# Kernel tuning notes

Measured on AMD Instinct MI355X. Metric: run time of the kernel, lower is better.

The kernel has to match this reference:

```python
import jax, jax.numpy as jnp
import numpy as np

B, N, H, W = 64, 21, 128, 128
MSE_WEIGHT = 1.0
SOFT_PCK_WEIGHT = 1.0


def setup_inputs() -> dict:
    key = jax.random.key(0)
    k1, k2, k3 = jax.random.split(key, 3)
    pred_heatmaps = jax.random.uniform(k1, (B, N, H, W), dtype=jnp.float32)
    gt_heatmaps = jax.random.uniform(k2, (B, N, H, W), dtype=jnp.float32)
    # pixel coordinates (x, y) in [0, W) x [0, H)
    gt_keypoints_2D = jax.random.uniform(k3, (B, N, 2), dtype=jnp.float32) * jnp.array([W, H], dtype=jnp.float32)
    return {"pred_heatmaps": pred_heatmaps, "gt_heatmaps": gt_heatmaps, "gt_keypoints_2D": gt_keypoints_2D}


def reference(pred_heatmaps, gt_heatmaps, gt_keypoints_2D):
    b, n, h, w = pred_heatmaps.shape
    # MSE over all elements
    mse_loss = jnp.mean((pred_heatmaps - gt_heatmaps) ** 2)
    # Vectorized keypoint gather: clamp coords, truncate-cast (matches torch .long())
    x = jnp.clip(gt_keypoints_2D[..., 0], 0, w - 1).astype(jnp.int32)  # (B, N)
    y = jnp.clip(gt_keypoints_2D[..., 1], 0, h - 1).astype(jnp.int32)  # (B, N)
    bi = jnp.arange(b)[:, None]
    ni = jnp.arange(n)[None, :]
    pred_vals = pred_heatmaps[bi, ni, y, x]  # (B, N)
    soft_pck_loss = jnp.sum((1.0 - pred_vals) ** 2) / (b * n)
    total_loss = MSE_WEIGHT * mse_loss + SOFT_PCK_WEIGHT * soft_pck_loss
    return (total_loss, mse_loss, soft_pck_loss)
```

## Files before the change

### kernel.cpp

```cpp
#include <hip/hip_runtime.h>

#define BB 64
#define NN 21
#define HH 128
#define WW 128
static constexpr long long TOT_ELEMS = (long long)BB * NN * HH * WW;
static constexpr int NV4 = (int)(TOT_ELEMS / 4);
static constexpr int NKP = BB * NN;

__global__ __launch_bounds__(256) void combined_loss_kernel(
    const float4* __restrict__ pred4,
    const float4* __restrict__ gt4,
    const float*  __restrict__ pred,
    const float*  __restrict__ kp,
    float* __restrict__ acc)
{
    const int tid    = blockIdx.x * blockDim.x + threadIdx.x;
    const int stride = gridDim.x * blockDim.x;

    float s = 0.0f;
    for (int i = tid; i < NV4; i += stride) {
        float4 p = pred4[i];
        float4 g = gt4[i];
        float d0 = p.x - g.x;
        float d1 = p.y - g.y;
        float d2 = p.z - g.z;
        float d3 = p.w - g.w;
        s += d0 * d0 + d1 * d1 + d2 * d2 + d3 * d3;
    }

    float s2 = 0.0f;
    if (tid < NKP) {
        float px = kp[2 * tid + 0];
        float py = kp[2 * tid + 1];
        int xi = (int)fminf(fmaxf(px, 0.0f), (float)(WW - 1));
        int yi = (int)fminf(fmaxf(py, 0.0f), (float)(HH - 1));
        float v = pred[(long long)tid * HH * WW + (long long)yi * WW + xi];
        float d = 1.0f - v;
        s2 = d * d;
    }

    #pragma unroll
    for (int off = 32; off > 0; off >>= 1) {
        s  += __shfl_down(s,  off, 64);
        s2 += __shfl_down(s2, off, 64);
    }

    __shared__ float ls[4], ls2[4];
    const int lane = threadIdx.x & 63;
    const int wid  = threadIdx.x >> 6;
    if (lane == 0) { ls[wid] = s; ls2[wid] = s2; }
    __syncthreads();
    if (threadIdx.x == 0) {
        float t = 0.0f, t2 = 0.0f;
        #pragma unroll
        for (int i = 0; i < 4; ++i) { t += ls[i]; t2 += ls2[i]; }
        atomicAdd(&acc[0], t);
        if (t2 != 0.0f) atomicAdd(&acc[1], t2);
    }
}

__global__ void finalize_kernel(const float* __restrict__ acc,
                                float* __restrict__ out)
{
    const float mse = acc[0] / (float)TOT_ELEMS;
    const float pck = acc[1] / (float)NKP;
    out[0] = mse + pck;
    out[1] = mse;
    out[2] = pck;
}

extern "C" void kernel_launch(void* const* d_in, const int* in_sizes, int n_in,
                              void* d_out, int out_size, void* d_ws, size_t ws_size,
                              hipStream_t stream) {
    const float* pred = (const float*)d_in[0];
    const float* gt   = (const float*)d_in[1];
    const float* kp   = (const float*)d_in[2];
    float* out = (float*)d_out;
    float* acc = (float*)d_ws;

    hipMemsetAsync(acc, 0, 2 * sizeof(float), stream);

    const int threads = 256;
    const int blocks  = 1024;
    combined_loss_kernel<<<blocks, threads, 0, stream>>>(
        (const float4*)pred, (const float4*)gt, pred, kp, acc);

    finalize_kernel<<<1, 1, 0, stream>>>(acc, out);
}
```

Before: 193.4 us.

## Unroll streaming loop, double grid, replace atomics with two-pass partial reduction

The grid-stride MSE loop is unrolled four-way with independent accumulators so more global loads are in flight per thread, and the grid grows from 1024 to 2048 blocks. Per-block partial sums are written to a workspace array instead of accumulated with atomics, which removes the memset launch. A 256-thread final kernel then reduces the partials and computes the outputs. This aims to hide memory latency in a bandwidth-bound reduction, at the cost of more registers and a workspace dependency of 16 KB.

```diff
diff --git a/kernel.cpp b/kernel.cpp
--- a/kernel.cpp
+++ b/kernel.cpp
@@ -8,26 +8,48 @@
 static constexpr int NV4 = (int)(TOT_ELEMS / 4);
 static constexpr int NKP = BB * NN;
 
-__global__ __launch_bounds__(256) void combined_loss_kernel(
+static constexpr int BLOCKS  = 2048;
+static constexpr int THREADS = 256;
+
+__global__ __launch_bounds__(THREADS) void combined_loss_partial(
     const float4* __restrict__ pred4,
     const float4* __restrict__ gt4,
     const float*  __restrict__ pred,
     const float*  __restrict__ kp,
-    float* __restrict__ acc)
+    float2* __restrict__ partial)
 {
     const int tid    = blockIdx.x * blockDim.x + threadIdx.x;
     const int stride = gridDim.x * blockDim.x;
 
-    float s = 0.0f;
-    for (int i = tid; i < NV4; i += stride) {
+    float s0 = 0.0f, s1 = 0.0f, s2a = 0.0f, s3 = 0.0f;
+    int i = tid;
+    for (; i + 3 * stride < NV4; i += 4 * stride) {
+        float4 p0 = pred4[i];
+        float4 p1 = pred4[i + stride];
+        float4 p2 = pred4[i + 2 * stride];
+        float4 p3 = pred4[i + 3 * stride];
+        float4 g0 = gt4[i];
+        float4 g1 = gt4[i + stride];
+        float4 g2 = gt4[i + 2 * stride];
+        float4 g3 = gt4[i + 3 * stride];
+        float d;
+        d = p0.x - g0.x; s0 += d * d;  d = p0.y - g0.y; s0 += d * d;
+        d = p0.z - g0.z; s0 += d * d;  d = p0.w - g0.w; s0 += d * d;
+        d = p1.x - g1.x; s1 += d * d;  d = p1.y - g1.y; s1 += d * d;
+        d = p1.z - g1.z; s1 += d * d;  d = p1.w - g1.w; s1 += d * d;
+        d = p2.x - g2.x; s2a += d * d; d = p2.y - g2.y; s2a += d * d;
+        d = p2.z - g2.z; s2a += d * d; d = p2.w - g2.w; s2a += d * d;
+        d = p3.x - g3.x; s3 += d * d;  d = p3.y - g3.y; s3 += d * d;
+        d = p3.z - g3.z; s3 += d * d;  d = p3.w - g3.w; s3 += d * d;
+    }
+    for (; i < NV4; i += stride) {
         float4 p = pred4[i];
         float4 g = gt4[i];
-        float d0 = p.x - g.x;
-        float d1 = p.y - g.y;
-        float d2 = p.z - g.z;
-        float d3 = p.w - g.w;
-        s += d0 * d0 + d1 * d1 + d2 * d2 + d3 * d3;
+        float d;
+        d = p.x - g.x; s0 += d * d;  d = p.y - g.y; s0 += d * d;
+        d = p.z - g.z; s0 += d * d;  d = p.w - g.w; s0 += d * d;
     }
+    float s = (s0 + s1) + (s2a + s3);
 
     float s2 = 0.0f;
     if (tid < NKP) {
@@ -36,8 +58,8 @@
         int xi = (int)fminf(fmaxf(px, 0.0f), (float)(WW - 1));
         int yi = (int)fminf(fmaxf(py, 0.0f), (float)(HH - 1));
         float v = pred[(long long)tid * HH * WW + (long long)yi * WW + xi];
-        float d = 1.0f - v;
-        s2 = d * d;
+        float dd = 1.0f - v;
+        s2 = dd * dd;
     }
 
     #pragma unroll
@@ -52,22 +74,40 @@
     if (lane == 0) { ls[wid] = s; ls2[wid] = s2; }
     __syncthreads();
     if (threadIdx.x == 0) {
-        float t = 0.0f, t2 = 0.0f;
-        #pragma unroll
-        for (int i = 0; i < 4; ++i) { t += ls[i]; t2 += ls2[i]; }
-        atomicAdd(&acc[0], t);
-        if (t2 != 0.0f) atomicAdd(&acc[1], t2);
+        float t  = (ls[0] + ls[1]) + (ls[2] + ls[3]);
+        float t2 = (ls2[0] + ls2[1]) + (ls2[2] + ls2[3]);
+        partial[blockIdx.x] = make_float2(t, t2);
     }
 }
 
-__global__ void finalize_kernel(const float* __restrict__ acc,
-                                float* __restrict__ out)
+__global__ __launch_bounds__(THREADS) void combined_loss_final(
+    const float2* __restrict__ partial,
+    float* __restrict__ out)
 {
-    const float mse = acc[0] / (float)TOT_ELEMS;
-    const float pck = acc[1] / (float)NKP;
-    out[0] = mse + pck;
-    out[1] = mse;
-    out[2] = pck;
+    float s = 0.0f, s2 = 0.0f;
+    for (int i = threadIdx.x; i < BLOCKS; i += THREADS) {
+        float2 p = partial[i];
+        s += p.x; s2 += p.y;
+    }
+    #pragma unroll
+    for (int off = 32; off > 0; off >>= 1) {
+        s  += __shfl_down(s,  off, 64);
+        s2 += __shfl_down(s2, off, 64);
+    }
+    __shared__ float ls[4], ls2[4];
+    const int lane = threadIdx.x & 63;
+    const int wid  = threadIdx.x >> 6;
+    if (lane == 0) { ls[wid] = s; ls2[wid] = s2; }
+    __syncthreads();
+    if (threadIdx.x == 0) {
+        float t  = (ls[0] + ls[1]) + (ls[2] + ls[3]);
+        float t2 = (ls2[0] + ls2[1]) + (ls2[2] + ls2[3]);
+        float mse = t / (float)TOT_ELEMS;
+        float pck = t2 / (float)NKP;
+        out[0] = mse + pck;
+        out[1] = mse;
+        out[2] = pck;
+    }
 }
 
 extern "C" void kernel_launch(void* const* d_in, const int* in_sizes, int n_in,
@@ -77,14 +117,10 @@
     const float* gt   = (const float*)d_in[1];
     const float* kp   = (const float*)d_in[2];
     float* out = (float*)d_out;
-    float* acc = (float*)d_ws;
+    float2* partial = (float2*)d_ws;
 
-    hipMemsetAsync(acc, 0, 2 * sizeof(float), stream);
+    combined_loss_partial<<<BLOCKS, THREADS, 0, stream>>>(
+        (const float4*)pred, (const float4*)gt, pred, kp, partial);
 
-    const int threads = 256;
-    const int blocks  = 1024;
-    combined_loss_kernel<<<blocks, threads, 0, stream>>>(
-        (const float4*)pred, (const float4*)gt, pred, kp, acc);
-
-    finalize_kernel<<<1, 1, 0, stream>>>(acc, out);
+    combined_loss_final<<<1, THREADS, 0, stream>>>(partial, out);
 }
```

New measurement: 195.2 us. No clear change (+1.0%).
